# Performance work log

Hardware: AMD Instinct MI355X
Metric: run time of the kernel (lower is better)

Reference implementation:

```python
import jax, jax.numpy as jnp
import numpy as np

EPS = 1e-5
PDIM, QKD, DIM = 64, 16, 256
SCALE = QKD ** -0.5


def setup_inputs() -> dict:
    key = jax.random.key(0)
    ks = jax.random.split(key, 13)
    B, H, W = 8, 64, 64
    return {
        "x": jax.random.normal(ks[0], (B, DIM, H, W), jnp.float32),
        "gn_g": jax.random.uniform(ks[1], (PDIM,), jnp.float32, 0.5, 1.5),
        "gn_b": jax.random.normal(ks[2], (PDIM,), jnp.float32) * 0.1,
        "qkv_w": jax.random.normal(ks[3], (2 * QKD + PDIM, PDIM), jnp.float32) * (PDIM ** -0.5),
        "qkv_bn_g": jax.random.uniform(ks[4], (2 * QKD + PDIM,), jnp.float32, 0.5, 1.5),
        "qkv_bn_b": jax.random.normal(ks[5], (2 * QKD + PDIM,), jnp.float32) * 0.1,
        "qkv_rm": jax.random.normal(ks[6], (2 * QKD + PDIM,), jnp.float32) * 0.1,
        "qkv_rv": jax.random.uniform(ks[7], (2 * QKD + PDIM,), jnp.float32, 0.5, 1.5),
        "proj_w": jax.random.normal(ks[8], (DIM, DIM), jnp.float32) * (DIM ** -0.5),
        "proj_bn_g": jax.random.uniform(ks[9], (DIM,), jnp.float32, 0.5, 1.5),
        "proj_bn_b": jax.random.normal(ks[10], (DIM,), jnp.float32) * 0.1,
        "proj_rm": jax.random.normal(ks[11], (DIM,), jnp.float32) * 0.1,
        "proj_rv": jax.random.uniform(ks[12], (DIM,), jnp.float32, 0.5, 1.5),
    }


def _bn(y, g, b, rm, rv):
    # inference BatchNorm over channel axis 1 of [B,C,H,W]
    inv = g / jnp.sqrt(rv + EPS)
    return y * inv[None, :, None, None] + (b - rm * inv)[None, :, None, None]


def reference(x, gn_g, gn_b, qkv_w, qkv_bn_g, qkv_bn_b, qkv_rm, qkv_rv,
              proj_w, proj_bn_g, proj_bn_b, proj_rm, proj_rv):
    B, C, H, W = x.shape
    x1, x2 = x[:, :PDIM], x[:, PDIM:]
    # GroupNorm with 1 group: normalize over (C,H,W) per sample
    mu = jnp.mean(x1, axis=(1, 2, 3), keepdims=True)
    var = jnp.var(x1, axis=(1, 2, 3), keepdims=True)
    x1n = (x1 - mu) / jnp.sqrt(var + EPS)
    x1n = x1n * gn_g[None, :, None, None] + gn_b[None, :, None, None]
    # qkv: 1x1 conv + BN
    qkv = jnp.einsum('bchw,oc->bohw', x1n, qkv_w)
    qkv = _bn(qkv, qkv_bn_g, qkv_bn_b, qkv_rm, qkv_rv)
    q, k, v = qkv[:, :QKD], qkv[:, QKD:2 * QKD], qkv[:, 2 * QKD:]
    N = H * W
    q = q.reshape(B, QKD, N)
    k = k.reshape(B, QKD, N)
    v = v.reshape(B, PDIM, N)
    attn = jnp.einsum('bcn,bcm->bnm', q, k) * SCALE  # [B,N,N]
    attn = jax.nn.softmax(attn, axis=-1)
    x1_attn = jnp.einsum('bcm,bnm->bcn', v, attn).reshape(B, PDIM, H, W)
    xc = jnp.concatenate([x1_attn, x2], axis=1)
    # proj: ReLU -> 1x1 conv -> BN
    y = jnp.einsum('bchw,oc->bohw', jax.nn.relu(xc), proj_w)
    return _bn(y, proj_bn_g, proj_bn_b, proj_rm, proj_rv)
```

## Files before the change

### kernel.cpp

```cpp
#include <hip/hip_runtime.h>
#include <hip/hip_bf16.h>

typedef __bf16 bf16;
typedef __bf16 bf16x4 __attribute__((ext_vector_type(4)));
typedef __bf16 bf16x8 __attribute__((ext_vector_type(8)));
typedef float  f32x16 __attribute__((ext_vector_type(16)));

#define MFMA32 __builtin_amdgcn_mfma_f32_32x32x16_bf16
#define EPSV 1e-5f
#define QSCALE 0.36067376022224085f

__device__ __forceinline__ f32x16 fzero16() {
  f32x16 z;
#pragma unroll
  for (int i = 0; i < 16; ++i) z[i] = 0.f;
  return z;
}

__device__ __forceinline__ void dma16(const void* g, void* s) {
  __builtin_amdgcn_global_load_lds(
      (const __attribute__((address_space(1))) void*)g,
      (__attribute__((address_space(3))) void*)s, 16, 0, 0);
}

__global__ __launch_bounds__(256) void k_stats_partial(const float* __restrict__ x,
                                                       float* __restrict__ part) {
  const int b = blockIdx.x >> 5, k = blockIdx.x & 31;
  const float* p = x + (size_t)b * 256 * 4096 + k * 8192;
  const int t = threadIdx.x;
  float s = 0.f, q = 0.f;
#pragma unroll
  for (int j = 0; j < 8; ++j) {
    float4 v = ((const float4*)p)[t + j * 256];
    s += v.x + v.y + v.z + v.w;
    q += v.x * v.x + v.y * v.y + v.z * v.z + v.w * v.w;
  }
  __shared__ float ls[256], lq[256];
  ls[t] = s; lq[t] = q;
  __syncthreads();
  for (int off = 128; off > 0; off >>= 1) {
    if (t < off) { ls[t] += ls[t + off]; lq[t] += lq[t + off]; }
    __syncthreads();
  }
  if (t == 0) { part[blockIdx.x * 2] = ls[0]; part[blockIdx.x * 2 + 1] = lq[0]; }
}

__global__ __launch_bounds__(256) void k_stats_final(const float* __restrict__ part,
                                                     float* __restrict__ stats) {
  const int t = threadIdx.x, b = t >> 5, k = t & 31;
  float s = part[(b * 32 + k) * 2], q = part[(b * 32 + k) * 2 + 1];
  for (int off = 16; off > 0; off >>= 1) {
    s += __shfl_down(s, off, 32);
    q += __shfl_down(q, off, 32);
  }
  if (k == 0) {
    const float inv_n = 1.f / 262144.f;
    const float mu = s * inv_n;
    const float var = q * inv_n - mu * mu;
    stats[b * 2] = mu;
    stats[b * 2 + 1] = rsqrtf(var + EPSV);
  }
}

__global__ __launch_bounds__(256) void k_qkv(
    const float* __restrict__ x, const float* __restrict__ gn_g, const float* __restrict__ gn_b,
    const float* __restrict__ qkv_w, const float* __restrict__ bn_g, const float* __restrict__ bn_b,
    const float* __restrict__ bn_rm, const float* __restrict__ bn_rv,
    const float* __restrict__ stats,
    bf16* __restrict__ qw, bf16* __restrict__ kw, bf16* __restrict__ vw) {
  const int b = blockIdx.x >> 6, tile = blockIdx.x & 63;
  const int n0 = tile * 64, t = threadIdx.x;
  __shared__ float xn[64][68];
  __shared__ float W[64][96];
  __shared__ float beta_s[96];
  const float mu = stats[b * 2], rstd = stats[b * 2 + 1];
  {
    const int c = t >> 2, f = t & 3;
    const float A = rstd * gn_g[c], B = gn_b[c] - mu * A;
    const float* xr = x + ((size_t)b * 256 + c) * 4096 + n0;
#pragma unroll
    for (int j = 0; j < 4; ++j) {
      float4 v = ((const float4*)xr)[f * 4 + j];
      const int nb = f * 16 + j * 4;
      xn[c][nb + 0] = v.x * A + B; xn[c][nb + 1] = v.y * A + B;
      xn[c][nb + 2] = v.z * A + B; xn[c][nb + 3] = v.w * A + B;
    }
  }
  for (int oc = t; oc < 96 * 8; oc += 256) {
    const int o = oc >> 3, ch = (oc & 7) * 8;
    const float inv = bn_g[o] * rsqrtf(bn_rv[o] + EPSV);
    if (ch == 0) beta_s[o] = bn_b[o] - bn_rm[o] * inv;
    const float* wr = qkv_w + o * 64 + ch;
#pragma unroll
    for (int i = 0; i < 8; ++i) W[ch + i][o] = wr[i] * inv;
  }
  __syncthreads();
  const int o_l = t & 31, ng = t >> 5;
#pragma unroll 1
  for (int p = 0; p < 3; ++p) {
    const int o = p * 32 + o_l;
    float acc[8];
#pragma unroll
    for (int j = 0; j < 8; ++j) acc[j] = 0.f;
    for (int c = 0; c < 64; ++c) {
      const float wv = W[c][o];
      const float* xr = &xn[c][ng * 8];
#pragma unroll
      for (int j = 0; j < 8; ++j) acc[j] += wv * xr[j];
    }
    const float beta = beta_s[o];
    const int nb = n0 + ng * 8;
    if (p == 0) {
      if (o < 16) {
#pragma unroll
        for (int j = 0; j < 8; ++j)
          qw[((size_t)b * 4096 + nb + j) * 16 + o] = (bf16)((acc[j] + beta) * QSCALE);
      } else {
#pragma unroll
        for (int j = 0; j < 8; ++j)
          kw[((size_t)b * 4096 + nb + j) * 16 + (o - 16)] = (bf16)(acc[j] + beta);
      }
    } else {
      const int c = (p - 1) * 32 + o_l;
      const int IT = nb >> 5;
      const int m4 = nb & 31;
      const int f  = ((m4 >> 4) << 1) + (c >> 5);
      const int b3 = (m4 >> 3) & 1;
      char* base = (char*)vw + (size_t)b * 524288 + (size_t)IT * 4096 +
                   f * 1024 + (c & 31) * 16 + b3 * 8;
      bf16x4 pk0, pk1;
#pragma unroll
      for (int i = 0; i < 4; ++i) {
        pk0[i] = (bf16)(acc[i] + beta);
        pk1[i] = (bf16)(acc[4 + i] + beta);
      }
      *(bf16x4*)base = pk0;
      *(bf16x4*)(base + 512) = pk1;
    }
  }
}

__global__ __launch_bounds__(256, 4) void k_attn(
    const bf16* __restrict__ qw, const bf16* __restrict__ kw,
    const bf16* __restrict__ vw, const float* __restrict__ x,
    bf16* __restrict__ xc) {
  __shared__ __align__(16) char smem[40960];
  const int orig = blockIdx.x;
  const int wg = (orig & 7) * 128 + (orig >> 3);
  const int b = wg >> 7, qblk = wg & 127;
  const int t = threadIdx.x;
  const int wid = t >> 6, l = t & 63, ln = l & 31, g = l >> 5;
  const int m0 = wid * 1024;

  const bf16* qb = qw + (size_t)b * 4096 * 16;
  const char* kb = (const char*)(kw + (size_t)b * 4096 * 16);
  const char* vfb = (const char*)vw + (size_t)b * 524288;

  const char* kdma = kb + (size_t)m0 * 32 + (2 * ln + g) * 16;
  const char* vdma = vfb + (size_t)(m0 >> 5) * 4096 + l * 16;
  char* ring = smem + wid * 10240;

  const int nq = qblk * 32 + ln;
  const bf16x8 qf = *(const bf16x8*)(qb + (size_t)nq * 16 + g * 8);
  asm volatile("" :: "v"(qf));

  f32x16 O0 = fzero16(), O1 = fzero16();
  float l_run = 0.f;

#pragma unroll
  for (int pt = 0; pt < 2; ++pt) {
    char* dst = ring + pt * 5120;
    const char* ks = kdma + (size_t)pt * 1024;
    const char* vs = vdma + (size_t)pt * 4096;
    dma16(ks, dst);
    dma16(vs, dst + 1024);
    dma16(vs + 1024, dst + 2048);
    dma16(vs + 2048, dst + 3072);
    dma16(vs + 3072, dst + 4096);
  }

#pragma unroll 1
  for (int it = 0; it < 32; ++it) {
    if (it < 31) { asm volatile("s_waitcnt vmcnt(5)" ::: "memory"); }
    else         { asm volatile("s_waitcnt vmcnt(0)" ::: "memory"); }
    const char* rb = ring + (it & 1) * 5120 + l * 16;
    const uint4 kc = *(const uint4*)rb;
    const uint4 v0 = *(const uint4*)(rb + 1024);
    const uint4 v1 = *(const uint4*)(rb + 2048);
    const uint4 v2 = *(const uint4*)(rb + 3072);
    const uint4 v3 = *(const uint4*)(rb + 4096);
    f32x16 S = MFMA32(__builtin_bit_cast(bf16x8, kc), qf, fzero16(), 0, 0, 0);
    float ts = 0.f;
#pragma unroll
    for (int r = 0; r < 16; ++r) { S[r] = __builtin_amdgcn_exp2f(S[r]); ts += S[r]; }
    l_run += ts;
    bf16x8 pb0, pb1;
#pragma unroll
    for (int r = 0; r < 8; ++r) { pb0[r] = (bf16)S[r]; pb1[r] = (bf16)S[r + 8]; }
    O0 = MFMA32(__builtin_bit_cast(bf16x8, v0), pb0, O0, 0, 0, 0);
    O1 = MFMA32(__builtin_bit_cast(bf16x8, v1), pb0, O1, 0, 0, 0);
    O0 = MFMA32(__builtin_bit_cast(bf16x8, v2), pb1, O0, 0, 0, 0);
    O1 = MFMA32(__builtin_bit_cast(bf16x8, v3), pb1, O1, 0, 0, 0);
    asm volatile("s_waitcnt lgkmcnt(0)" ::: "memory");
    if (it + 2 < 32) {
      char* dst = ring + (it & 1) * 5120;
      const char* ks = kdma + (size_t)(it + 2) * 1024;
      const char* vs = vdma + (size_t)(it + 2) * 4096;
      dma16(ks, dst);
      dma16(vs, dst + 1024);
      dma16(vs + 1024, dst + 2048);
      dma16(vs + 2048, dst + 3072);
      dma16(vs + 3072, dst + 4096);
    }
  }
  l_run += __shfl_xor(l_run, 32, 64);

  __syncthreads();

  {
    char* orow = smem + wid * 4096 + ln * 128;
    const int msk = 2 * (ln & 7);
#pragma unroll
    for (int h = 0; h < 2; ++h) {
      const f32x16& O = h ? O1 : O0;
#pragma unroll
      for (int j = 0; j < 4; ++j) {
        bf16x4 e;
#pragma unroll
        for (int i = 0; i < 4; ++i) e[i] = (bf16)O[4 * j + i];
        const int chunk = h * 8 + 2 * j + g;
        *(bf16x4*)(orow + ((chunk ^ msk) << 3)) = e;
      }
    }
    if (g == 0) *(float*)(smem + 16384 + wid * 128 + ln * 4) = l_run;
  }
  __syncthreads();

  {
    const int n = t >> 3, k8 = t & 7;
    const int off = ((2 * k8) ^ (2 * (n & 7))) << 3;
    float L = 0.f;
    float acc[8];
#pragma unroll
    for (int e = 0; e < 8; ++e) acc[e] = 0.f;
#pragma unroll
    for (int kr_ = 0; kr_ < 4; ++kr_) {
      L += *(const float*)(smem + 16384 + kr_ * 128 + n * 4);
      const bf16x8 v = *(const bf16x8*)(smem + kr_ * 4096 + n * 128 + off);
#pragma unroll
      for (int e = 0; e < 8; ++e) acc[e] += (float)v[e];
    }
    const float rL = 1.0f / L;
    bf16x8 o8;
#pragma unroll
    for (int e = 0; e < 8; ++e) o8[e] = (bf16)fmaxf(acc[e] * rL, 0.f);
    *(bf16x8*)(xc + ((size_t)b * 4096 + qblk * 32 + n) * 256 + k8 * 8) = o8;
  }
  __syncthreads();

  {
    unsigned* tile_u = (unsigned*)smem;
    const float* xb = x + ((size_t)b * 256 + 64) * 4096 + qblk * 32;
#pragma unroll
    for (int i = 0; i < 3; ++i) {
      const int idx = i * 256 + t;
      const int cp = idx >> 3, f = idx & 7;
      const float4 a = *(const float4*)(xb + (size_t)(2 * cp) * 4096 + f * 4);
      const float4 c4 = *(const float4*)(xb + (size_t)(2 * cp + 1) * 4096 + f * 4);
      const float av[4] = {a.x, a.y, a.z, a.w};
      const float cv[4] = {c4.x, c4.y, c4.z, c4.w};
#pragma unroll
      for (int e = 0; e < 4; ++e) {
        const unsigned u =
            (unsigned)__builtin_bit_cast(unsigned short, (bf16)fmaxf(av[e], 0.f)) |
            ((unsigned)__builtin_bit_cast(unsigned short, (bf16)fmaxf(cv[e], 0.f)) << 16);
        tile_u[(f * 4 + e) * 97 + cp] = u;
      }
    }
    __syncthreads();
#pragma unroll
    for (int i = 0; i < 3; ++i) {
      const int idx = i * 256 + t;
      const int n = idx / 24, q = idx % 24;
      const uint4 d = *(const uint4*)&tile_u[n * 97 + q * 4];
      *(uint4*)(xc + ((size_t)b * 4096 + qblk * 32 + n) * 256 + 64 + q * 8) = d;
    }
  }
}

__global__ __launch_bounds__(256, 2) void k_proj(
    const bf16* __restrict__ xc, const float* __restrict__ pw,
    const float* __restrict__ bn_g, const float* __restrict__ bn_b,
    const float* __restrict__ bn_rm, const float* __restrict__ bn_rv,
    float* __restrict__ out) {
  const int orig = blockIdx.x;
  const int wg = (orig & 7) * 64 + (orig >> 3);
  const int b = wg >> 6, rem = wg & 63, nt = rem >> 1, oh = rem & 1;
  const int n0 = nt * 128, o0 = oh * 128;
  const int t = threadIdx.x, w = t >> 6, l = t & 63, ln = l & 31, g = l >> 5;

  __shared__ __align__(16) bf16 pws[128 * 256];
  __shared__ float beta_s[128];

  {
    const int o = t >> 1, half = t & 1;
    const float inv = bn_g[o0 + o] * rsqrtf(bn_rv[o0 + o] + EPSV);
    if (half == 0) beta_s[o] = bn_b[o0 + o] - bn_rm[o0 + o] * inv;
    const float* wr = pw + (size_t)(o0 + o) * 256 + half * 128;
    const int s_hh = (o & 15) * 8;
#pragma unroll
    for (int j = 0; j < 16; ++j) {
      const float4 a = ((const float4*)wr)[j * 2];
      const float4 c4 = ((const float4*)wr)[j * 2 + 1];
      bf16x8 v8;
      v8[0] = (bf16)(a.x * inv);  v8[1] = (bf16)(a.y * inv);
      v8[2] = (bf16)(a.z * inv);  v8[3] = (bf16)(a.w * inv);
      v8[4] = (bf16)(c4.x * inv); v8[5] = (bf16)(c4.y * inv);
      v8[6] = (bf16)(c4.z * inv); v8[7] = (bf16)(c4.w * inv);
      *(bf16x8*)&pws[o * 256 + ((half * 128 + j * 8) ^ s_hh)] = v8;
    }
  }
  __syncthreads();

  const bf16* xrow = xc + ((size_t)b * 4096 + n0 + w * 32 + ln) * 256;
  const int sw = (ln & 15) * 8;
  f32x16 acc0 = fzero16(), acc1 = fzero16(), acc2 = fzero16(), acc3 = fzero16();
#pragma unroll 4
  for (int ck = 0; ck < 256; ck += 16) {
    const bf16x8 bfrag = *(const bf16x8*)(xrow + ck + g * 8);
    const int cidx = (ck + g * 8) ^ sw;
    const bf16x8 a0 = *(const bf16x8*)&pws[(ln) * 256 + cidx];
    const bf16x8 a1 = *(const bf16x8*)&pws[(32 + ln) * 256 + cidx];
    const bf16x8 a2 = *(const bf16x8*)&pws[(64 + ln) * 256 + cidx];
    const bf16x8 a3 = *(const bf16x8*)&pws[(96 + ln) * 256 + cidx];
    acc0 = MFMA32(a0, bfrag, acc0, 0, 0, 0);
    acc1 = MFMA32(a1, bfrag, acc1, 0, 0, 0);
    acc2 = MFMA32(a2, bfrag, acc2, 0, 0, 0);
    acc3 = MFMA32(a3, bfrag, acc3, 0, 0, 0);
  }
  const int ncol = n0 + w * 32 + ln;
  float* ob = out + (size_t)b * 256 * 4096 + ncol;
#pragma unroll
  for (int og = 0; og < 4; ++og) {
    const f32x16& A = og == 0 ? acc0 : og == 1 ? acc1 : og == 2 ? acc2 : acc3;
#pragma unroll
    for (int r = 0; r < 16; ++r) {
      const int o_loc = og * 32 + (r & 3) + 8 * (r >> 2) + 4 * g;
      ob[(size_t)(o0 + o_loc) * 4096] = A[r] + beta_s[o_loc];
    }
  }
}

extern "C" void kernel_launch(void* const* d_in, const int* in_sizes, int n_in,
                              void* d_out, int out_size, void* d_ws, size_t ws_size,
                              hipStream_t stream) {
  (void)in_sizes; (void)n_in; (void)out_size; (void)ws_size;
  const float* x        = (const float*)d_in[0];
  const float* gn_g     = (const float*)d_in[1];
  const float* gn_b     = (const float*)d_in[2];
  const float* qkv_w    = (const float*)d_in[3];
  const float* qkv_bn_g = (const float*)d_in[4];
  const float* qkv_bn_b = (const float*)d_in[5];
  const float* qkv_rm   = (const float*)d_in[6];
  const float* qkv_rv   = (const float*)d_in[7];
  const float* proj_w   = (const float*)d_in[8];
  const float* proj_bn_g = (const float*)d_in[9];
  const float* proj_bn_b = (const float*)d_in[10];
  const float* proj_rm  = (const float*)d_in[11];
  const float* proj_rv  = (const float*)d_in[12];

  char* ws = (char*)d_ws;
  float* part  = (float*)ws;
  float* stats = (float*)(ws + 4096);
  bf16* qw = (bf16*)(ws + 8192);
  bf16* kw = (bf16*)(ws + 8192 + (1u << 20));
  bf16* vw = (bf16*)(ws + 8192 + (2u << 20));
  bf16* xc = (bf16*)(ws + 8192 + (6u << 20));

  k_stats_partial<<<256, 256, 0, stream>>>(x, part);
  k_stats_final<<<1, 256, 0, stream>>>(part, stats);
  k_qkv<<<512, 256, 0, stream>>>(x, gn_g, gn_b, qkv_w, qkv_bn_g, qkv_bn_b,
                                 qkv_rm, qkv_rv, stats, qw, kw, vw);
  k_attn<<<1024, 256, 0, stream>>>(qw, kw, vw, x, xc);
  k_proj<<<512, 256, 0, stream>>>(xc, proj_w, proj_bn_g, proj_bn_b,
                                  proj_rm, proj_rv, (float*)d_out);
}
```

Baseline: 90.53 us.

## Process two 32-query tiles per attention block to reuse K/V loads

```diff
diff --git a/kernel.cpp b/kernel.cpp
--- a/kernel.cpp
+++ b/kernel.cpp
@@ -140,14 +140,14 @@
   }
 }
 
-__global__ __launch_bounds__(256, 4) void k_attn(
+__global__ __launch_bounds__(256, 2) void k_attn(
     const bf16* __restrict__ qw, const bf16* __restrict__ kw,
     const bf16* __restrict__ vw, const float* __restrict__ x,
     bf16* __restrict__ xc) {
   __shared__ __align__(16) char smem[40960];
   const int orig = blockIdx.x;
-  const int wg = (orig & 7) * 128 + (orig >> 3);
-  const int b = wg >> 7, qblk = wg & 127;
+  const int wg = (orig & 7) * 64 + (orig >> 3);
+  const int b = wg >> 6, qblk = wg & 63;
   const int t = threadIdx.x;
   const int wid = t >> 6, l = t & 63, ln = l & 31, g = l >> 5;
   const int m0 = wid * 1024;
@@ -160,12 +160,14 @@
   const char* vdma = vfb + (size_t)(m0 >> 5) * 4096 + l * 16;
   char* ring = smem + wid * 10240;
 
-  const int nq = qblk * 32 + ln;
-  const bf16x8 qf = *(const bf16x8*)(qb + (size_t)nq * 16 + g * 8);
-  asm volatile("" :: "v"(qf));
-
-  f32x16 O0 = fzero16(), O1 = fzero16();
-  float l_run = 0.f;
+  const int nq = qblk * 64 + ln;
+  const bf16x8 qf0 = *(const bf16x8*)(qb + (size_t)nq * 16 + g * 8);
+  const bf16x8 qf1 = *(const bf16x8*)(qb + (size_t)(nq + 32) * 16 + g * 8);
+  asm volatile("" :: "v"(qf0), "v"(qf1));
+
+  f32x16 O00 = fzero16(), O01 = fzero16();
+  f32x16 O10 = fzero16(), O11 = fzero16();
+  float l0 = 0.f, l1 = 0.f;
 
 #pragma unroll
   for (int pt = 0; pt < 2; ++pt) {
@@ -189,18 +191,29 @@
     const uint4 v1 = *(const uint4*)(rb + 2048);
     const uint4 v2 = *(const uint4*)(rb + 3072);
     const uint4 v3 = *(const uint4*)(rb + 4096);
-    f32x16 S = MFMA32(__builtin_bit_cast(bf16x8, kc), qf, fzero16(), 0, 0, 0);
-    float ts = 0.f;
-#pragma unroll
-    for (int r = 0; r < 16; ++r) { S[r] = __builtin_amdgcn_exp2f(S[r]); ts += S[r]; }
-    l_run += ts;
-    bf16x8 pb0, pb1;
-#pragma unroll
-    for (int r = 0; r < 8; ++r) { pb0[r] = (bf16)S[r]; pb1[r] = (bf16)S[r + 8]; }
-    O0 = MFMA32(__builtin_bit_cast(bf16x8, v0), pb0, O0, 0, 0, 0);
-    O1 = MFMA32(__builtin_bit_cast(bf16x8, v1), pb0, O1, 0, 0, 0);
-    O0 = MFMA32(__builtin_bit_cast(bf16x8, v2), pb1, O0, 0, 0, 0);
-    O1 = MFMA32(__builtin_bit_cast(bf16x8, v3), pb1, O1, 0, 0, 0);
+    const bf16x8 kf = __builtin_bit_cast(bf16x8, kc);
+    f32x16 S0 = MFMA32(kf, qf0, fzero16(), 0, 0, 0);
+    f32x16 S1 = MFMA32(kf, qf1, fzero16(), 0, 0, 0);
+    float ts0 = 0.f, ts1 = 0.f;
+#pragma unroll
+    for (int r = 0; r < 16; ++r) { S0[r] = __builtin_amdgcn_exp2f(S0[r]); ts0 += S0[r]; }
+#pragma unroll
+    for (int r = 0; r < 16; ++r) { S1[r] = __builtin_amdgcn_exp2f(S1[r]); ts1 += S1[r]; }
+    l0 += ts0; l1 += ts1;
+    bf16x8 pa0, pa1, pc0, pc1;
+#pragma unroll
+    for (int r = 0; r < 8; ++r) {
+      pa0[r] = (bf16)S0[r]; pa1[r] = (bf16)S0[r + 8];
+      pc0[r] = (bf16)S1[r]; pc1[r] = (bf16)S1[r + 8];
+    }
+    O00 = MFMA32(__builtin_bit_cast(bf16x8, v0), pa0, O00, 0, 0, 0);
+    O10 = MFMA32(__builtin_bit_cast(bf16x8, v0), pc0, O10, 0, 0, 0);
+    O01 = MFMA32(__builtin_bit_cast(bf16x8, v1), pa0, O01, 0, 0, 0);
+    O11 = MFMA32(__builtin_bit_cast(bf16x8, v1), pc0, O11, 0, 0, 0);
+    O00 = MFMA32(__builtin_bit_cast(bf16x8, v2), pa1, O00, 0, 0, 0);
+    O10 = MFMA32(__builtin_bit_cast(bf16x8, v2), pc1, O10, 0, 0, 0);
+    O01 = MFMA32(__builtin_bit_cast(bf16x8, v3), pa1, O01, 0, 0, 0);
+    O11 = MFMA32(__builtin_bit_cast(bf16x8, v3), pc1, O11, 0, 0, 0);
     asm volatile("s_waitcnt lgkmcnt(0)" ::: "memory");
     if (it + 2 < 32) {
       char* dst = ring + (it & 1) * 5120;
@@ -213,58 +226,66 @@
       dma16(vs + 3072, dst + 4096);
     }
   }
-  l_run += __shfl_xor(l_run, 32, 64);
+  l0 += __shfl_xor(l0, 32, 64);
+  l1 += __shfl_xor(l1, 32, 64);
 
   __syncthreads();
 
   {
-    char* orow = smem + wid * 4096 + ln * 128;
     const int msk = 2 * (ln & 7);
 #pragma unroll
-    for (int h = 0; h < 2; ++h) {
-      const f32x16& O = h ? O1 : O0;
-#pragma unroll
-      for (int j = 0; j < 4; ++j) {
-        bf16x4 e;
-#pragma unroll
-        for (int i = 0; i < 4; ++i) e[i] = (bf16)O[4 * j + i];
-        const int chunk = h * 8 + 2 * j + g;
-        *(bf16x4*)(orow + ((chunk ^ msk) << 3)) = e;
+    for (int hq = 0; hq < 2; ++hq) {
+      char* orow = smem + (wid * 2 + hq) * 4096 + ln * 128;
+#pragma unroll
+      for (int hc = 0; hc < 2; ++hc) {
+        const f32x16& O = hq ? (hc ? O11 : O10) : (hc ? O01 : O00);
+#pragma unroll
+        for (int j = 0; j < 4; ++j) {
+          bf16x4 e;
+#pragma unroll
+          for (int i = 0; i < 4; ++i) e[i] = (bf16)O[4 * j + i];
+          const int chunk = hc * 8 + 2 * j + g;
+          *(bf16x4*)(orow + ((chunk ^ msk) << 3)) = e;
+        }
       }
-    }
-    if (g == 0) *(float*)(smem + 16384 + wid * 128 + ln * 4) = l_run;
+      if (g == 0) *(float*)(smem + 32768 + (wid * 2 + hq) * 128 + ln * 4) = hq ? l1 : l0;
+    }
   }
   __syncthreads();
 
   {
     const int n = t >> 3, k8 = t & 7;
     const int off = ((2 * k8) ^ (2 * (n & 7))) << 3;
-    float L = 0.f;
-    float acc[8];
-#pragma unroll
-    for (int e = 0; e < 8; ++e) acc[e] = 0.f;
-#pragma unroll
-    for (int kr_ = 0; kr_ < 4; ++kr_) {
-      L += *(const float*)(smem + 16384 + kr_ * 128 + n * 4);
-      const bf16x8 v = *(const bf16x8*)(smem + kr_ * 4096 + n * 128 + off);
-#pragma unroll
-      for (int e = 0; e < 8; ++e) acc[e] += (float)v[e];
-    }
-    const float rL = 1.0f / L;
-    bf16x8 o8;
-#pragma unroll
-    for (int e = 0; e < 8; ++e) o8[e] = (bf16)fmaxf(acc[e] * rL, 0.f);
-    *(bf16x8*)(xc + ((size_t)b * 4096 + qblk * 32 + n) * 256 + k8 * 8) = o8;
+#pragma unroll
+    for (int hq = 0; hq < 2; ++hq) {
+      float L = 0.f;
+      float acc[8];
+#pragma unroll
+      for (int e = 0; e < 8; ++e) acc[e] = 0.f;
+#pragma unroll
+      for (int kr_ = 0; kr_ < 4; ++kr_) {
+        const int s = kr_ * 2 + hq;
+        L += *(const float*)(smem + 32768 + s * 128 + n * 4);
+        const bf16x8 v = *(const bf16x8*)(smem + s * 4096 + n * 128 + off);
+#pragma unroll
+        for (int e = 0; e < 8; ++e) acc[e] += (float)v[e];
+      }
+      const float rL = 1.0f / L;
+      bf16x8 o8;
+#pragma unroll
+      for (int e = 0; e < 8; ++e) o8[e] = (bf16)fmaxf(acc[e] * rL, 0.f);
+      *(bf16x8*)(xc + ((size_t)b * 4096 + qblk * 64 + hq * 32 + n) * 256 + k8 * 8) = o8;
+    }
   }
   __syncthreads();
 
   {
     unsigned* tile_u = (unsigned*)smem;
-    const float* xb = x + ((size_t)b * 256 + 64) * 4096 + qblk * 32;
-#pragma unroll
-    for (int i = 0; i < 3; ++i) {
+    const float* xb = x + ((size_t)b * 256 + 64) * 4096 + qblk * 64;
+#pragma unroll
+    for (int i = 0; i < 6; ++i) {
       const int idx = i * 256 + t;
-      const int cp = idx >> 3, f = idx & 7;
+      const int cp = idx >> 4, f = idx & 15;
       const float4 a = *(const float4*)(xb + (size_t)(2 * cp) * 4096 + f * 4);
       const float4 c4 = *(const float4*)(xb + (size_t)(2 * cp + 1) * 4096 + f * 4);
       const float av[4] = {a.x, a.y, a.z, a.w};
@@ -279,11 +300,11 @@
     }
     __syncthreads();
 #pragma unroll
-    for (int i = 0; i < 3; ++i) {
+    for (int i = 0; i < 6; ++i) {
       const int idx = i * 256 + t;
       const int n = idx / 24, q = idx % 24;
       const uint4 d = *(const uint4*)&tile_u[n * 97 + q * 4];
-      *(uint4*)(xc + ((size_t)b * 4096 + qblk * 32 + n) * 256 + 64 + q * 8) = d;
+      *(uint4*)(xc + ((size_t)b * 4096 + qblk * 64 + n) * 256 + 64 + q * 8) = d;
     }
   }
 }
@@ -381,7 +402,7 @@
   k_stats_final<<<1, 256, 0, stream>>>(part, stats);
   k_qkv<<<512, 256, 0, stream>>>(x, gn_g, gn_b, qkv_w, qkv_bn_g, qkv_bn_b,
                                  qkv_rm, qkv_rv, stats, qw, kw, vw);
-  k_attn<<<1024, 256, 0, stream>>>(qw, kw, vw, x, xc);
+  k_attn<<<512, 256, 0, stream>>>(qw, kw, vw, x, xc);
   k_proj<<<512, 256, 0, stream>>>(xc, proj_w, proj_bn_g, proj_bn_b,
                                   proj_rm, proj_rv, (float*)d_out);
 }
```

Result: faster. 87.48 us (-3.4%).
